# Performance work log

Hardware: AMD Instinct MI355X
Metric: run time of the kernel (lower is better)

Reference implementation:

```python
import jax, jax.numpy as jnp
import numpy as np
import math

D_HEAD = 64  # scaling uses sqrt(d_head), NOT sqrt of full projection dim (faithful to source)

def setup_inputs() -> dict:
    key = jax.random.key(0)
    ks = jax.random.split(key, 9)
    B, S, D = 4, 2048, 1024
    s = 0.02
    return {
        "x": jax.random.normal(ks[0], (B, S, D), dtype=jnp.float32),
        "Wq": jax.random.normal(ks[1], (D, D), dtype=jnp.float32) * s,
        "bq": jax.random.normal(ks[2], (D,), dtype=jnp.float32) * s,
        "Wk": jax.random.normal(ks[3], (D, D), dtype=jnp.float32) * s,
        "bk": jax.random.normal(ks[4], (D,), dtype=jnp.float32) * s,
        "Wv": jax.random.normal(ks[5], (D, D), dtype=jnp.float32) * s,
        "bv": jax.random.normal(ks[6], (D,), dtype=jnp.float32) * s,
        "Wo": jax.random.normal(ks[7], (D, D), dtype=jnp.float32) * s,
        "bo": jax.random.normal(ks[8], (D,), dtype=jnp.float32) * s,
    }

def reference(x, Wq, bq, Wk, bk, Wv, bv, Wo, bo):
    # Q/K/V projections: [B,S,D] @ [D,D] + b
    Q = jnp.einsum('bsd,de->bse', x, Wq) + bq
    K = jnp.einsum('bsd,de->bse', x, Wk) + bk
    V = jnp.einsum('bsd,de->bse', x, Wv) + bv
    # NOTE: source does bmm over the FULL projected dim (no head split),
    # scaled by sqrt(d_head) only.
    scores = jnp.einsum('bqd,bkd->bqk', Q, K) / math.sqrt(D_HEAD)  # [B,S,S]
    S_len = scores.shape[-1]
    causal = jnp.tril(jnp.ones((S_len, S_len), dtype=bool))
    scores = jnp.where(causal, scores, -jnp.inf)
    weights = jax.nn.softmax(scores, axis=-1)
    attn_out = jnp.einsum('bqk,bkd->bqd', weights, V)
    return jnp.einsum('bsd,de->bse', attn_out, Wo) + bo
```

## Files before the change

### kernel.cpp

```cpp
#include <hip/hip_runtime.h>
#include <stdint.h>

typedef _Float16 f16;
typedef __attribute__((ext_vector_type(8))) _Float16 f16x8;
typedef __attribute__((ext_vector_type(4))) _Float16 f16x4;
typedef __attribute__((ext_vector_type(4))) float f32x4;

#define BK 32

typedef __attribute__((address_space(3))) uint32_t lds_u32;
typedef const __attribute__((address_space(1))) uint32_t glb_u32;

__device__ __forceinline__ void gload_lds16(const void* g, void* l) {
    __builtin_amdgcn_global_load_lds((glb_u32*)g, (lds_u32*)l, 16, 0, 0);
}

template<int OUT_MODE, int CAUSAL, int TM, int TN>
__device__ __forceinline__
void gemm_body(const f16* __restrict__ A, const f16* __restrict__ B,
               const float* __restrict__ bias, const float* __restrict__ bias2,
               void* __restrict__ Cv, void* __restrict__ C2,
               int M, int N, int K,
               long long sAb, long long sBb, long long sCb, float scale,
               int bx, int by, int bzi)
{
    constexpr int IM = TM / 32;
    constexpr int JN = TN / 32;

    int mtile, n0;
    if (CAUSAL == 1) {
        int rem = bx, mi = 0;
        while (rem > mi) { rem -= mi + 1; ++mi; }
        mtile = mi;
        n0 = rem * TN;
    } else {
        mtile = by;
        n0 = bx * TN;
    }

    const int tid  = threadIdx.x;
    const int wave = tid >> 6;
    const int lane = tid & 63;
    const long long bz = bzi;
    A += bz * sAb;
    B += bz * sBb;

    __shared__ f16 As[TM * BK];
    __shared__ f16 Bs[TN * BK];

    const int srow  = lane >> 2;
    const int scolS = (((lane & 3) ^ ((srow >> 1) & 3))) * 8;
    const int fr    = lane & 15;
    const int fkS   = (((lane >> 4) ^ ((fr >> 1) & 3))) * 8;

    const int wm = (wave >> 1) * (TM / 2);
    const int wn = (wave & 1) * (TN / 2);

    const int npass = (CAUSAL == 2) ? 2 : 1;
    for (int pass = 0; pass < npass; ++pass) {
        const int mt = (CAUSAL == 2 && pass == 1) ? (M / TM - 1 - mtile) : mtile;
        const int m0 = mt * TM;
        const int Kend = (CAUSAL == 2) ? (m0 + TM) : K;

        f32x4 acc[IM][JN] = {};

        for (int k0 = 0; k0 < Kend; k0 += BK) {
            #pragma unroll
            for (int gg = 0; gg < TM / 64; ++gg) {
                const int g = wave * (TM / 64) + gg;
                gload_lds16(A + (long long)(m0 + g * 16 + srow) * K + (k0 + scolS),
                            &As[g * 512]);
            }
            #pragma unroll
            for (int gg = 0; gg < TN / 64; ++gg) {
                const int g = wave * (TN / 64) + gg;
                gload_lds16(B + (long long)(n0 + g * 16 + srow) * K + (k0 + scolS),
                            &Bs[g * 512]);
            }
            __syncthreads();

            f16x8 af[IM], bf[JN];
            #pragma unroll
            for (int i = 0; i < IM; ++i)
                af[i] = *(const f16x8*)&As[(wm + i * 16 + fr) * BK + fkS];
            #pragma unroll
            for (int j = 0; j < JN; ++j)
                bf[j] = *(const f16x8*)&Bs[(wn + j * 16 + fr) * BK + fkS];

            #pragma unroll
            for (int i = 0; i < IM; ++i)
                #pragma unroll
                for (int j = 0; j < JN; ++j)
                    acc[i][j] = __builtin_amdgcn_mfma_f32_16x16x32_f16(af[i], bf[j], acc[i][j], 0, 0, 0);
            __syncthreads();
        }

        const int cn = lane & 15;
        const int cm = (lane >> 4) * 4;
        #pragma unroll
        for (int j = 0; j < JN; ++j) {
            const int gn = n0 + wn + j * 16 + cn;
            #pragma unroll
            for (int i = 0; i < IM; ++i) {
                const int gm = m0 + wm + i * 16 + cm;
                if (OUT_MODE == 0) {
                    const float bv = bias ? bias[gn] : 0.f;
                    float* C = (float*)Cv + bz * sCb;
                    #pragma unroll
                    for (int r = 0; r < 4; ++r)
                        C[(long long)(gm + r) * N + gn] = acc[i][j][r] * scale + bv;
                } else if (OUT_MODE == 1) {
                    const float bv = bias ? bias[(long long)bz * N + gn] : 0.f;
                    f16* C = (f16*)Cv + bz * sCb;
                    #pragma unroll
                    for (int r = 0; r < 4; ++r)
                        C[(long long)(gm + r) * N + gn] = (f16)(acc[i][j][r] * scale + bv);
                } else {
                    const int sel = gn >> 10;
                    const int nn  = gn & 1023;
                    if (sel == 0) {
                        f16* C = (f16*)Cv;
                        #pragma unroll
                        for (int r = 0; r < 4; ++r)
                            C[(long long)(gm + r) * 1024 + nn] = (f16)acc[i][j][r];
                    } else {
                        const float bb = bias2[nn];
                        f16* C = (f16*)C2;
                        const int b = gm >> 11, s = gm & 2047;
                        f16x4 pk;
                        #pragma unroll
                        for (int r = 0; r < 4; ++r)
                            pk[r] = (f16)(acc[i][j][r] + bb);
                        *(f16x4*)&C[(long long)b * 2097152 + (long long)nn * 2048 + s] = pk;
                    }
                }
            }
        }
        if (CAUSAL == 2) __syncthreads();
    }
}

template<int OUT_MODE, int CAUSAL, int TM, int TN>
__global__ __launch_bounds__(256, 2)
void gemm_bt(const f16* __restrict__ A, const f16* __restrict__ B,
             const float* __restrict__ bias, const float* __restrict__ bias2,
             void* __restrict__ Cv, void* __restrict__ C2,
             int M, int N, int K,
             long long sAb, long long sBb, long long sCb, float scale)
{
    gemm_body<OUT_MODE, CAUSAL, TM, TN>(A, B, bias, bias2, Cv, C2, M, N, K,
                                        sAb, sBb, sCb, scale,
                                        blockIdx.x, blockIdx.y, blockIdx.z);
}

__global__ __launch_bounds__(256)
void prep(const float* __restrict__ x,  const float* __restrict__ Wq,
          const float* __restrict__ bq, const float* __restrict__ Wk,
          const float* __restrict__ Wv, const float* __restrict__ bv,
          const float* __restrict__ Wo,
          f16* __restrict__ xb,  f16* __restrict__ Wqf, f16* __restrict__ Wkf,
          f16* __restrict__ Wvf, f16* __restrict__ Wot,
          float* __restrict__ bvo, float* __restrict__ wvec)
{
    __shared__ f16 tile[32][33];
    __shared__ float red[4][64];
    const int t = threadIdx.x;
    int id = blockIdx.x;

    if (id < 8192) {
        const int i = (id * 256 + t) * 4;
        const float4 v = *(const float4*)&x[i];
        f16x4 o; o[0]=(f16)v.x; o[1]=(f16)v.y; o[2]=(f16)v.z; o[3]=(f16)v.w;
        *(f16x4*)&xb[i] = o;
        return;
    }
    id -= 8192;
    if (id < 3072) {
        const float* src = (id < 1024) ? Wq : (id < 2048) ? Wk : Wv;
        f16* dst = (id < 1024) ? Wqf : (id < 2048) ? Wkf : Wvf;
        const int i = ((id & 1023) * 256 + t) * 4;
        const float4 v = *(const float4*)&src[i];
        f16x4 o; o[0]=(f16)v.x; o[1]=(f16)v.y; o[2]=(f16)v.z; o[3]=(f16)v.w;
        *(f16x4*)&dst[i] = o;
        return;
    }
    id -= 3072;
    if (id < 1024) {
        const int bx = (id & 31) * 32, by = (id >> 5) * 32;
        const int tx = t & 31, ty = t >> 5;
        #pragma unroll
        for (int i = 0; i < 32; i += 8)
            tile[ty + i][tx] = (f16)Wo[(long long)(by + ty + i) * 1024 + (bx + tx)];
        __syncthreads();
        #pragma unroll
        for (int i = 0; i < 32; i += 8)
            Wot[(long long)(bx + ty + i) * 1024 + (by + tx)] = tile[tx][ty + i];
        return;
    }
    id -= 1024;
    if (id < 16) {
        const int e0 = id * 64;
        const int wave = t >> 6, lane = t & 63;
        float acc = 0.f;
        for (int i = 0; i < 256; ++i) {
            const int k = wave * 256 + i;
            acc += bv[k] * Wo[(long long)k * 1024 + e0 + lane];
        }
        red[wave][lane] = acc;
        __syncthreads();
        if (wave == 0)
            bvo[e0 + lane] = red[0][lane] + red[1][lane] + red[2][lane] + red[3][lane];
        return;
    }
    id -= 16;
    {
        const int row = id * 4 + (t >> 6);
        const int lane = t & 63;
        const float* src = Wk + (long long)row * 1024;
        float a = 0.f;
        #pragma unroll
        for (int tt = 0; tt < 16; ++tt) a += src[lane + 64 * tt] * bq[lane + 64 * tt];
        #pragma unroll
        for (int o = 32; o > 0; o >>= 1) a += __shfl_down(a, o);
        if (lane == 0) wvec[row] = a * 0.125f;
    }
}

__global__ __launch_bounds__(256, 2)
void dual_weights_cvec(const f16* __restrict__ Wkf, const f16* __restrict__ Wqf,
                       const f16* __restrict__ Wot, const f16* __restrict__ Wvf,
                       f16* __restrict__ Wcat2,
                       const f16* __restrict__ xb, const float* __restrict__ wvec,
                       float* __restrict__ cbias)
{
    if (blockIdx.z == 2) {
        const int flat = blockIdx.y * 16 + blockIdx.x;
        const int wave = threadIdx.x >> 6, lane = threadIdx.x & 63;
        #pragma unroll
        for (int rr = 0; rr < 8; ++rr) {
            const int row = (flat * 4 + wave) * 8 + rr;
            const f16* src = xb + (long long)row * 1024;
            float a = 0.f;
            #pragma unroll
            for (int tt = 0; tt < 16; ++tt)
                a += (float)src[lane + 64 * tt] * wvec[lane + 64 * tt];
            #pragma unroll
            for (int o = 32; o > 0; o >>= 1) a += __shfl_down(a, o);
            if (lane == 0) cbias[row] = a;
        }
        return;
    }
    const f16* Ax = (blockIdx.z == 0) ? Wkf : Wot;
    const f16* Bx = (blockIdx.z == 0) ? Wqf : Wvf;
    f16* Cx = Wcat2 + (long long)blockIdx.z * 1024 * 1024;
    gemm_body<1, 0, 64, 64>(Ax, Bx, nullptr, nullptr, Cx, nullptr,
                            1024, 1024, 1024, 0, 0, 0, 1.f,
                            blockIdx.x, blockIdx.y, 0);
}

__global__ __launch_bounds__(256)
void softmax_causal(const f16* __restrict__ Sc, f16* __restrict__ P, int S)
{
    const long long row = blockIdx.x;
    const int q = (int)(row % S);
    const f16* src = Sc + row * S;
    f16* dst = P + row * S;
    const int t = threadIdx.x;
    __shared__ float redm[4], reds[4];

    f16x8 vv = {};
    if (t * 8 <= q) vv = *(const f16x8*)&src[t * 8];
    float v[8];
    float mx = -3.0e38f;
    #pragma unroll
    for (int i = 0; i < 8; ++i) {
        const int k = t * 8 + i;
        v[i] = (float)vv[i];
        if (k <= q) mx = fmaxf(mx, v[i]);
    }
    #pragma unroll
    for (int o = 32; o > 0; o >>= 1) mx = fmaxf(mx, __shfl_down(mx, o));
    if ((t & 63) == 0) redm[t >> 6] = mx;
    __syncthreads();
    mx = fmaxf(fmaxf(redm[0], redm[1]), fmaxf(redm[2], redm[3]));

    float sum = 0.f;
    #pragma unroll
    for (int i = 0; i < 8; ++i) {
        const int k = t * 8 + i;
        v[i] = (k <= q) ? __expf(v[i] - mx) : 0.f;
        sum += v[i];
    }
    #pragma unroll
    for (int o = 32; o > 0; o >>= 1) sum += __shfl_down(sum, o);
    if ((t & 63) == 0) reds[t >> 6] = sum;
    __syncthreads();
    sum = reds[0] + reds[1] + reds[2] + reds[3];
    const float inv = 1.f / sum;
    f16x8 ov;
    #pragma unroll
    for (int i = 0; i < 8; ++i) ov[i] = (f16)(v[i] * inv);
    *(f16x8*)&dst[t * 8] = ov;
}

extern "C" void kernel_launch(void* const* d_in, const int* in_sizes, int n_in,
                              void* d_out, int out_size, void* d_ws, size_t ws_size,
                              hipStream_t stream)
{
    const float* x  = (const float*)d_in[0];
    const float* Wq = (const float*)d_in[1];
    const float* bq = (const float*)d_in[2];
    const float* Wk = (const float*)d_in[3];
    const float* Wv = (const float*)d_in[5];
    const float* bv = (const float*)d_in[6];
    const float* Wo = (const float*)d_in[7];
    const float* bo = (const float*)d_in[8];
    float* out = (float*)d_out;

    const int B = 4, S = 2048, D = 1024;
    const long long SD  = (long long)S * D;
    const long long SS  = (long long)S * S;
    const long long BSD = (long long)B * SD;
    const int MS = B * S;

    char* p = (char*)d_ws;
    f16*   xb    = (f16*)p;  p += BSD * 2;
    f16*   Wqf   = (f16*)p;  p += (long long)D * D * 2;
    f16*   Wkf   = (f16*)p;  p += (long long)D * D * 2;
    f16*   Wvf   = (f16*)p;  p += (long long)D * D * 2;
    f16*   Wot   = (f16*)p;  p += (long long)D * D * 2;
    f16*   Wcat2 = (f16*)p;  p += 2LL * D * D * 2;
    float* bvo   = (float*)p; p += D * 4;
    float* wvec  = (float*)p; p += D * 4;
    float* cbias = (float*)p; p += (long long)MS * 4;
    f16*   Qh    = (f16*)p;  p += BSD * 2;
    f16*   Vt    = (f16*)p;  p += BSD * 2;
    f16*   Sc    = (f16*)p;  p += (long long)B * SS * 2;
    f16*   Pb    = (f16*)p;  p += (long long)B * SS * 2;

    dim3 blk(256);

    prep<<<dim3(12560), blk, 0, stream>>>(x, Wq, bq, Wk, Wv, bv, Wo,
                                          xb, Wqf, Wkf, Wvf, Wot, bvo, wvec);

    dual_weights_cvec<<<dim3(16, 16, 3), blk, 0, stream>>>(Wkf, Wqf, Wot, Wvf,
                                                           Wcat2, xb, wvec, cbias);

    dim3 gproj(2 * D / 128, MS / 128, 1);
    gemm_bt<3, 0, 128, 128><<<gproj, blk, 0, stream>>>(xb, Wcat2, nullptr, bvo,
                                                       Qh, Vt,
                                                       MS, 2 * D, D, 0, 0, 0, 1.f);

    dim3 gsc(136, 1, B);
    gemm_bt<1, 1, 128, 128><<<gsc, blk, 0, stream>>>(Qh, xb, cbias, nullptr,
                                                     Sc, nullptr,
                                                     S, S, D, SD, SD, SS, 0.125f);

    softmax_causal<<<dim3((unsigned)(B * S)), blk, 0, stream>>>(Sc, Pb, S);

    dim3 gpv(D / 64, S / 128 / 2, B);
    gemm_bt<0, 2, 128, 64><<<gpv, blk, 0, stream>>>(Pb, Vt, bo, nullptr,
                                                    out, nullptr,
                                                    S, D, S, SS, SD, SD, 1.f);
}
```

Before: 278.8 us.

## Add 256x256-tile 8-wave projection GEMM with phased LDS pipelining

Replaces the 128x128 generic projection GEMM with a dedicated kernel that uses 256x256 output tiles, 512 threads and a BK of 64. Loads go directly from global memory to LDS with an XOR swizzle, split into four phases per k-step so they overlap the MFMA work. Workgroup order is remapped so that consecutive blocks share operand tiles in cache. The larger tiles are meant to raise arithmetic intensity and reduce global traffic for the projection stage, at the cost of 128KB of LDS per block and fewer blocks in flight. The hand-written waitcnt and barrier sequencing is fragile if the counts are wrong.

```diff
diff --git a/kernel.cpp b/kernel.cpp
--- a/kernel.cpp
+++ b/kernel.cpp
@@ -153,6 +153,142 @@
                                         blockIdx.x, blockIdx.y, blockIdx.z);
 }
 
+
+__device__ __forceinline__
+void stage_half(const f16* __restrict__ G, int ldg, f16* lds_half,
+                int grow0, int k0, int tid)
+{
+    const int lr  = tid >> 3;
+    const int csw = ((tid & 7) * 8) ^ ((lr & 7) << 3);
+    gload_lds16(G + (long long)(grow0 + lr) * ldg + (k0 + csw),
+                lds_half + ((tid >> 6) << 9));
+    gload_lds16(G + (long long)(grow0 + 64 + lr) * ldg + (k0 + csw),
+                lds_half + 4096 + ((tid >> 6) << 9));
+}
+
+__global__ __launch_bounds__(512, 2)
+void gemm_proj_8ph(const f16* __restrict__ A, const f16* __restrict__ B,
+                   const float* __restrict__ bvo,
+                   f16* __restrict__ Qh, f16* __restrict__ Vt,
+                   int M, int N, int K)
+{
+    (void)M;
+    __shared__ f16 As[2][16384];
+    __shared__ f16 Bs[2][16384];
+
+    const int nwg  = gridDim.x;
+    const int orig = blockIdx.x;
+    const int swz  = (orig & 7) * (nwg >> 3) + (orig >> 3);
+    const int ntn  = N >> 8;
+    const int mt = swz / ntn, nt = swz - mt * ntn;
+    const int m0 = mt << 8, n0 = nt << 8;
+
+    const int tid  = threadIdx.x;
+    const int lane = tid & 63;
+    const int wave = tid >> 6;
+    const int wm = (wave >> 2) << 7;
+    const int wn = (wave & 3) << 6;
+    const int fr  = lane & 15;
+    const int hk  = lane >> 4;
+    const int lsw = lane & 7;
+    const int nkt = K >> 6;
+
+    f32x4 acc[8][4] = {};
+    f16x8 bf[4][2];
+
+    stage_half(A, K, &As[0][0],    m0,       0, tid);
+    stage_half(A, K, &As[0][8192], m0 + 128, 0, tid);
+    stage_half(B, K, &Bs[0][0],    n0,       0, tid);
+    stage_half(B, K, &Bs[0][8192], n0 + 128, 0, tid);
+    if (nkt > 1) {
+        stage_half(B, K, &Bs[1][0],    n0,       64, tid);
+        stage_half(B, K, &Bs[1][8192], n0 + 128, 64, tid);
+        asm volatile("s_waitcnt vmcnt(4)" ::: "memory");
+    } else {
+        asm volatile("s_waitcnt vmcnt(0)" ::: "memory");
+    }
+    __builtin_amdgcn_s_barrier();
+
+    for (int t = 0; t < nkt; ++t) {
+        const f16* Ab = As[t & 1];
+        const f16* Bb = Bs[t & 1];
+        #pragma unroll
+        for (int p = 0; p < 4; ++p) {
+            if (p == 0) {
+                #pragma unroll
+                for (int j = 0; j < 4; ++j)
+                    #pragma unroll
+                    for (int kk = 0; kk < 2; ++kk)
+                        bf[j][kk] = *(const f16x8*)((const char*)Bb +
+                            ((wn + j * 16 + fr) << 7) +
+                            ((((kk << 2) | hk) ^ lsw) << 4));
+            }
+            f16x8 af[2][2];
+            #pragma unroll
+            for (int ii = 0; ii < 2; ++ii)
+                #pragma unroll
+                for (int kk = 0; kk < 2; ++kk)
+                    af[ii][kk] = *(const f16x8*)((const char*)Ab +
+                        ((wm + (2 * p + ii) * 16 + fr) << 7) +
+                        ((((kk << 2) | hk) ^ lsw) << 4));
+
+            if (p == 0 && t + 1 < nkt)
+                stage_half(A, K, &As[(t + 1) & 1][0],    m0,       (t + 1) << 6, tid);
+            if (p == 1 && t + 1 < nkt)
+                stage_half(A, K, &As[(t + 1) & 1][8192], m0 + 128, (t + 1) << 6, tid);
+            if (p == 2 && t + 2 < nkt)
+                stage_half(B, K, &Bs[t & 1][0],          n0,       (t + 2) << 6, tid);
+            if (p == 3 && t + 2 < nkt)
+                stage_half(B, K, &Bs[t & 1][8192],       n0 + 128, (t + 2) << 6, tid);
+
+            if (p == 0) asm volatile("s_waitcnt lgkmcnt(8)" ::: "memory");
+            __builtin_amdgcn_s_barrier();
+            asm volatile("s_waitcnt lgkmcnt(0)" ::: "memory");
+            __builtin_amdgcn_s_setprio(1);
+            #pragma unroll
+            for (int ii = 0; ii < 2; ++ii)
+                #pragma unroll
+                for (int j = 0; j < 4; ++j)
+                    #pragma unroll
+                    for (int kk = 0; kk < 2; ++kk)
+                        acc[2 * p + ii][j] = __builtin_amdgcn_mfma_f32_16x16x32_f16(
+                            af[ii][kk], bf[j][kk], acc[2 * p + ii][j], 0, 0, 0);
+            __builtin_amdgcn_s_setprio(0);
+            if (p == 3) {
+                if (t + 2 < nkt) asm volatile("s_waitcnt vmcnt(4)" ::: "memory");
+                else             asm volatile("s_waitcnt vmcnt(0)" ::: "memory");
+            }
+            __builtin_amdgcn_s_barrier();
+        }
+    }
+
+    const int cn  = lane & 15;
+    const int cm4 = (lane >> 4) * 4;
+    #pragma unroll
+    for (int j = 0; j < 4; ++j) {
+        const int gn  = n0 + wn + j * 16 + cn;
+        const int sel = gn >> 10;
+        const int nn  = gn & 1023;
+        #pragma unroll
+        for (int i = 0; i < 8; ++i) {
+            const int gm = m0 + wm + i * 16 + cm4;
+            if (sel == 0) {
+                #pragma unroll
+                for (int r = 0; r < 4; ++r)
+                    Qh[(long long)(gm + r) * 1024 + nn] = (f16)acc[i][j][r];
+            } else {
+                const float bb = bvo[nn];
+                const int b = gm >> 11, s = gm & 2047;
+                f16x4 pk;
+                #pragma unroll
+                for (int r = 0; r < 4; ++r)
+                    pk[r] = (f16)(acc[i][j][r] + bb);
+                *(f16x4*)&Vt[(long long)b * 2097152 + (long long)nn * 2048 + s] = pk;
+            }
+        }
+    }
+}
+
 __global__ __launch_bounds__(256)
 void prep(const float* __restrict__ x,  const float* __restrict__ Wq,
           const float* __restrict__ bq, const float* __restrict__ Wk,
@@ -346,10 +482,9 @@
     dual_weights_cvec<<<dim3(16, 16, 3), blk, 0, stream>>>(Wkf, Wqf, Wot, Wvf,
                                                            Wcat2, xb, wvec, cbias);
 
-    dim3 gproj(2 * D / 128, MS / 128, 1);
-    gemm_bt<3, 0, 128, 128><<<gproj, blk, 0, stream>>>(xb, Wcat2, nullptr, bvo,
-                                                       Qh, Vt,
-                                                       MS, 2 * D, D, 0, 0, 0, 1.f);
+    dim3 gproj((MS / 256) * (2 * D / 256));
+    gemm_proj_8ph<<<gproj, dim3(512), 0, stream>>>(xb, Wcat2, bvo, Qh, Vt,
+                                                   MS, 2 * D, D);
 
     dim3 gsc(136, 1, B);
     gemm_bt<1, 1, 128, 128><<<gsc, blk, 0, stream>>>(Qh, xb, cbias, nullptr,
```

Result: faster. 269.2 us (-3.4%).
